# Performance work log

Hardware: AMD Instinct MI355X
Metric: run time of the kernel (lower is better)

## Reference

```python
import jax, jax.numpy as jnp
import numpy as np

EPS = 1e-5
CROSS = 12  # cross_size


def bn(x, g, b):
    # inference BatchNorm2d with running_mean=0, running_var=1
    s = g / jnp.sqrt(1.0 + EPS)
    return x * s[None, :, None, None] + b[None, :, None, None]


def conv1x1(x, w, b=None):
    # w: [out_c, in_c]
    y = jnp.einsum('bchw,oc->bohw', x, w)
    if b is not None:
        y = y + b[None, :, None, None]
    return y


def mlp(x, w1, b1, w2, b2):
    # Mlp with channels_first=True: 1x1 conv -> GELU -> 1x1 conv (drop=0)
    return conv1x1(jax.nn.gelu(conv1x1(x, w1, b1), approximate=False), w2, b2)


def setup_inputs() -> dict:
    key = jax.random.key(0)
    ks = jax.random.split(key, 24)
    B, Cl, Ch = 8, 128, 64
    Hl = Wl = 96
    Hh = Wh = 192

    def w(k, o, i):
        return jax.random.normal(k, (o, i), jnp.float32) / np.float32(np.sqrt(i))

    return {
        'x_l': jax.random.normal(ks[0], (B, Cl, Hl, Wl), jnp.float32),
        'x_h': jax.random.normal(ks[1], (B, Ch, Hh, Wh), jnp.float32),
        # mlp_l (hidden = in = Cl)
        'mlp_l_w1': w(ks[2], Cl, Cl), 'mlp_l_b1': jnp.zeros((Cl,), jnp.float32),
        'mlp_l_w2': w(ks[3], Cl, Cl), 'mlp_l_b2': jnp.zeros((Cl,), jnp.float32),
        # conv_1x1(Cl->Ch) + BN + ReLU
        'conv_w': w(ks[4], Ch, Cl),
        'conv_bn_g': jnp.ones((Ch,), jnp.float32), 'conv_bn_b': jnp.zeros((Ch,), jnp.float32),
        # cross_kv: BN(Cl) -> AdaptiveMaxPool(12,12) -> Conv1x1(Cl -> 2*Ch)
        'kv_bn_g': jnp.ones((Cl,), jnp.float32), 'kv_bn_b': jnp.zeros((Cl,), jnp.float32),
        'kv_w': w(ks[5], 2 * Ch, Cl), 'kv_b': jnp.zeros((2 * Ch,), jnp.float32),
        # self.norm: BN(Ch)
        'norm_g': jnp.ones((Ch,), jnp.float32), 'norm_b': jnp.zeros((Ch,), jnp.float32),
        # mlp_h
        'mlp_h_w1': w(ks[6], Ch, Ch), 'mlp_h_b1': jnp.zeros((Ch,), jnp.float32),
        'mlp_h_w2': w(ks[7], Ch, Ch), 'mlp_h_b2': jnp.zeros((Ch,), jnp.float32),
    }


def reference(x_l, x_h,
              mlp_l_w1, mlp_l_b1, mlp_l_w2, mlp_l_b2,
              conv_w, conv_bn_g, conv_bn_b,
              kv_bn_g, kv_bn_b, kv_w, kv_b,
              norm_g, norm_b,
              mlp_h_w1, mlp_h_b1, mlp_h_w2, mlp_h_b2):
    B, Cl, Hl, Wl = x_l.shape
    _, Ch, Hh, Wh = x_h.shape
    S = CROSS * CROSS  # 144

    # x_l = x_l + mlp_l(x_l)
    x_l = x_l + mlp(x_l, mlp_l_w1, mlp_l_b1, mlp_l_w2, mlp_l_b2)

    # x_h = x_h + interpolate(conv(x_l))
    x_l_conv = jax.nn.relu(bn(conv1x1(x_l, conv_w), conv_bn_g, conv_bn_b))
    up = jax.image.resize(x_l_conv, (B, Ch, Hh, Wh), method='linear')
    x_h = x_h + up

    # cross_kv(x_l): BN -> adaptive max pool to 12x12 -> 1x1 conv to 2*Ch
    xn_l = bn(x_l, kv_bn_g, kv_bn_b)
    pooled = xn_l.reshape(B, Cl, CROSS, Hl // CROSS, CROSS, Wl // CROSS).max(axis=(3, 5))
    kv = conv1x1(pooled, kv_w, kv_b)              # [B, 2*Ch, 12, 12]
    k, v = kv[:, :Ch], kv[:, Ch:]                 # each [B, Ch, 12, 12]
    k_mat = k.transpose(0, 2, 3, 1).reshape(B, S, Ch)  # grouped-conv kernel [B,S,Ch]
    v_mat = v.reshape(B, Ch, S)                        # grouped-conv kernel [B,Ch,S]

    # attn_h
    xn_h = bn(x_h, norm_g, norm_b)                # [B,Ch,Hh,Wh]
    attn = jnp.einsum('bchw,bsc->bshw', xn_h, k_mat)  # [B,S,Hh,Wh]
    attn = jax.nn.softmax(attn * (S ** -0.5), axis=1)
    out = jnp.einsum('bshw,bcs->bchw', attn, v_mat)   # [B,Ch,Hh,Wh]
    x_h = x_h + out

    # x_h = x_h + mlp_h(x_h)
    x_h = x_h + mlp(x_h, mlp_h_w1, mlp_h_b1, mlp_h_w2, mlp_h_b2)
    return x_h
```

## Files before the change

kernel.cpp:

```cpp
#include <hip/hip_runtime.h>
#include <math.h>

#define NB 8
#define CL 128
#define CH 64
#define HL 96
#define WL 96
#define PL (HL*WL)
#define HH 192
#define WH 192
#define PH (HH*WH)
#define NS 144
#define BN_S 0.9999950000374997f
#define INV12 (1.0f/12.0f)

typedef __attribute__((ext_vector_type(8))) short bf16x8;
typedef __attribute__((ext_vector_type(4))) float f32x4;
typedef __attribute__((ext_vector_type(2))) unsigned int uu2;
#define MFMA16(a,b,c) __builtin_amdgcn_mfma_f32_16x16x32_bf16(a,b,c,0,0,0)

__device__ __forceinline__ float gelu_exact(float x){
    return 0.5f*x*(1.0f + erff(x*0.7071067811865475f));
}
__device__ __forceinline__ void st4(short* p, float a, float b, float c, float d){
    uu2 r;
    asm("v_cvt_pk_bf16_f32 %0, %1, %2" : "=v"(r.x) : "v"(a), "v"(b));
    asm("v_cvt_pk_bf16_f32 %0, %1, %2" : "=v"(r.y) : "v"(c), "v"(d));
    *(uu2*)p = r;
}
__device__ __forceinline__ void st4v(short* p, float4 v){ st4(p, v.x, v.y, v.z, v.w); }

__global__ __launch_bounds__(512) void k_mlp_l(
    const float* __restrict__ xl, const float* __restrict__ w1, const float* __restrict__ b1,
    const float* __restrict__ w2, const float* __restrict__ b2,
    const float* __restrict__ cw, const float* __restrict__ bng, const float* __restrict__ bnb,
    float* __restrict__ xl2, float* __restrict__ xc)
{
    __shared__ short Wb[128*136];
    __shared__ short Xb[64*136];
    __shared__ float bS[256];
    __shared__ float bC[128];
    const int tid = threadIdx.x;
    const int b   = blockIdx.x / (PL/64);
    const int hw0 = (blockIdx.x % (PL/64)) * 64;
    const float* xb = xl + (size_t)b*CL*PL + hw0;
    const int w = tid>>6, lane = tid&63, l16 = lane&15, q = lane>>4;
    const int g = w&3, h = w>>2;
    const int pw = g*16, px = pw + l16;
    #pragma unroll
    for (int i=0;i<8;i++){
        int idx4 = i*512+tid;
        int row = idx4>>5, c4 = (idx4&31)<<2;
        st4v(&Wb[row*136 + c4], *(const float4*)&w1[(row<<7) + c4]);
    }
    {
        const int p = tid&63, wv = tid>>6;
        #pragma unroll
        for (int i=0;i<4;i++){
            int c0 = wv*4 + i*32;
            float a0 = xb[(size_t)(c0+0)*PL + p];
            float a1 = xb[(size_t)(c0+1)*PL + p];
            float a2 = xb[(size_t)(c0+2)*PL + p];
            float a3 = xb[(size_t)(c0+3)*PL + p];
            st4(&Xb[p*136 + c0], a0,a1,a2,a3);
        }
    }
    if (tid < 128) bS[tid] = b1[tid]; else if (tid < 256) bS[tid] = b2[tid-128];
    if (tid < 64) bC[tid] = bng[tid]*BN_S; else if (tid < 128) bC[tid] = bnb[tid-64];
    __syncthreads();
    float hv[4][4];
    #pragma unroll
    for (int m2=0; m2<4; m2++){
        const int mt = h*4 + m2;
        f32x4 acc = {0.f,0.f,0.f,0.f};
        #pragma unroll
        for (int k=0;k<4;k++){
            bf16x8 af = *(const bf16x8*)&Wb[(mt*16+l16)*136 + k*32 + q*8];
            bf16x8 bf = *(const bf16x8*)&Xb[(pw+l16)*136 + k*32 + q*8];
            acc = MFMA16(af, bf, acc);
        }
        #pragma unroll
        for (int r=0;r<4;r++) hv[m2][r] = gelu_exact(acc[r] + bS[mt*16+q*4+r]);
    }
    __syncthreads();
    #pragma unroll
    for (int m2=0;m2<4;m2++)
        st4(&Xb[px*136 + (h*4+m2)*16 + q*4], hv[m2][0],hv[m2][1],hv[m2][2],hv[m2][3]);
    #pragma unroll
    for (int i=0;i<8;i++){
        int idx4 = i*512+tid;
        int row = idx4>>5, c4 = (idx4&31)<<2;
        st4v(&Wb[row*136 + c4], *(const float4*)&w2[(row<<7) + c4]);
    }
    __syncthreads();
    float* yb = xl2 + (size_t)b*CL*PL + hw0;
    #pragma unroll
    for (int m2=0; m2<4; m2++){
        const int mt = h*4 + m2;
        f32x4 acc = {0.f,0.f,0.f,0.f};
        #pragma unroll
        for (int k=0;k<4;k++){
            bf16x8 af = *(const bf16x8*)&Wb[(mt*16+l16)*136 + k*32 + q*8];
            bf16x8 bf = *(const bf16x8*)&Xb[(pw+l16)*136 + k*32 + q*8];
            acc = MFMA16(af, bf, acc);
        }
        #pragma unroll
        for (int r=0;r<4;r++){
            int o = mt*16 + q*4 + r;
            size_t off = (size_t)o*PL + px;
            float yy = acc[r] + bS[128+o] + xb[off];
            yb[off] = yy;
            hv[m2][r] = yy;
        }
    }
    __syncthreads();
    #pragma unroll
    for (int m2=0;m2<4;m2++)
        st4(&Xb[px*136 + (h*4+m2)*16 + q*4], hv[m2][0],hv[m2][1],hv[m2][2],hv[m2][3]);
    #pragma unroll
    for (int i=0;i<4;i++){
        int idx4 = i*512+tid;
        int row = idx4>>5, c4 = (idx4&31)<<2;
        st4v(&Wb[row*136 + c4], *(const float4*)&cw[(row<<7) + c4]);
    }
    __syncthreads();
    float* cb = xc + (size_t)b*CH*PL + hw0;
    #pragma unroll
    for (int m2=0; m2<2; m2++){
        const int mt = h*2 + m2;
        f32x4 acc = {0.f,0.f,0.f,0.f};
        #pragma unroll
        for (int k=0;k<4;k++){
            bf16x8 af = *(const bf16x8*)&Wb[(mt*16+l16)*136 + k*32 + q*8];
            bf16x8 bf = *(const bf16x8*)&Xb[(pw+l16)*136 + k*32 + q*8];
            acc = MFMA16(af, bf, acc);
        }
        #pragma unroll
        for (int r=0;r<4;r++){
            int o = mt*16 + q*4 + r;
            cb[(size_t)o*PL + px] = fmaxf(bC[o]*acc[r] + bC[64+o], 0.f);
        }
    }
}

__global__ __launch_bounds__(192) void k_pool(
    const float* __restrict__ xl2, const float* __restrict__ g, const float* __restrict__ bta,
    float* __restrict__ pooled)
{
    const int plane = blockIdx.x;
    const int tid = threadIdx.x;
    if (tid >= NS) return;
    const int c = plane & (CL-1);
    const float sc = g[c]*BN_S;
    const float tc = bta[c];
    const int i = tid/12, j = tid%12;
    const float* base = xl2 + (size_t)plane*PL + (size_t)i*8*WL + j*8;
    float m = -3.4e38f;
    #pragma unroll
    for (int dy=0;dy<8;dy++){
        float4 a = *(const float4*)(base + dy*WL);
        float4 bb = *(const float4*)(base + dy*WL + 4);
        float m0 = fmaxf(fmaxf(sc*a.x+tc, sc*a.y+tc), fmaxf(sc*a.z+tc, sc*a.w+tc));
        float m1 = fmaxf(fmaxf(sc*bb.x+tc, sc*bb.y+tc), fmaxf(sc*bb.z+tc, sc*bb.w+tc));
        m = fmaxf(m, fmaxf(m0, m1));
    }
    pooled[(size_t)plane*NS + tid] = m;
}

__global__ __launch_bounds__(256) void k_kv(
    const float* __restrict__ pooled, const float* __restrict__ kvw, const float* __restrict__ kvb,
    const float* __restrict__ ng, const float* __restrict__ nb,
    float* __restrict__ keg, float* __restrict__ vg, float* __restrict__ biasg)
{
    const int t = blockIdx.x*256 + threadIdx.x;
    const int s = t % NS;
    const int r = t / NS;
    const int o = r & 127;
    const int b = r >> 7;
    const float* P = pooled + (size_t)b*CL*NS + s;
    const float* W = kvw + (size_t)o*CL;
    float acc = kvb[o];
    #pragma unroll 4
    for (int c=0;c<CL;c++) acc = fmaf(W[c], P[(size_t)c*NS], acc);
    if (o < CH){
        keg[((size_t)b*NS+s)*CH + o] = acc * (ng[o]*(BN_S*INV12));
        atomicAdd(&biasg[b*NS+s], acc * (nb[o]*INV12));
    } else {
        vg[((size_t)b*CH + (o-CH))*NS + s] = acc;
    }
}

__global__ __launch_bounds__(256) void k_attn(
    const float* __restrict__ xh, const float* __restrict__ xc,
    const float* __restrict__ keg, const float* __restrict__ vg,
    const float* __restrict__ biasg,
    const float* __restrict__ w1h, const float* __restrict__ b1h,
    const float* __restrict__ w2h, const float* __restrict__ b2h,
    float* __restrict__ out)
{
    __shared__ short KP[64*168];
    __shared__ short VW[64*168];
    __shared__ short Xb[64*72];
    __shared__ float bS[NS];
    __shared__ float bH[128];
    const int tid = threadIdx.x;
    const int b   = blockIdx.x / (PH/64);
    const int hw0 = (blockIdx.x % (PH/64)) * 64;
    const int y   = hw0 / WH;
    const int xst = hw0 % WH;
    const int   lyr = (y>>1) - ((y&1)^1);
    const float fy  = (y&1) ? 0.25f : 0.75f;
    const int   y0i = lyr<0?0:lyr;
    const int   y1i = (lyr+1>HL-1)?(HL-1):(lyr+1);

    const float* xb  = xh + (size_t)b*CH*PH + hw0;
    const float* xcb = xc + (size_t)b*CH*PL;
    const float* keb = keg + (size_t)b*NS*CH;
    const float* vb  = vg + (size_t)b*CH*NS;

    const int w = tid>>6, lane = tid&63, l16 = lane&15, q = lane>>4;
    const int pw = w*16, px = pw + l16;

    #pragma unroll
    for (int i=0;i<9;i++){
        int idx4 = i*256+tid;
        int s = idx4>>4, c4 = (idx4&15)<<2;
        st4v(&KP[s*72 + c4], *(const float4*)&keb[(s<<6) + c4]);
    }
    #pragma unroll
    for (int i=0;i<9;i++){
        int idx4 = i*256+tid;
        int c = idx4/36, s4 = (idx4 - c*36)<<2;
        st4v(&VW[c*168 + s4], *(const float4*)&vb[c*NS + s4]);
    }
    { int row = tid>>2, o4 = (tid&3)<<2;
      *(uu2*)&VW[row*168 + 144 + o4] = (uu2){0u,0u}; }
    if (tid < NS) bS[tid] = biasg[b*NS+tid];
    if (tid < 64) bH[tid] = b1h[tid]; else if (tid < 128) bH[tid] = b2h[tid-64];

    const int xo  = xst + px;
    const int lx  = (xo>>1) - ((xo&1)^1);
    const float fx = (xo&1) ? 0.25f : 0.75f;
    const int x0i = lx<0?0:lx;
    const int x1i = (lx+1>WL-1)?(WL-1):(lx+1);
    float resid[16];
    #pragma unroll
    for (int mt=0; mt<4; mt++){
        #pragma unroll
        for (int r=0; r<4; r++){
            int ch = mt*16 + q*4 + r;
            const float* s = xcb + (size_t)ch*PL;
            float v00 = s[y0i*WL+x0i], v01 = s[y0i*WL+x1i];
            float v10 = s[y1i*WL+x0i], v11 = s[y1i*WL+x1i];
            float top = v00 + fx*(v01-v00);
            float bot = v10 + fx*(v11-v10);
            float up  = top + fy*(bot-top);
            resid[mt*4+r] = xb[(size_t)ch*PH + px] + up;
        }
        st4(&Xb[px*72 + mt*16 + q*4],
            resid[mt*4+0], resid[mt*4+1], resid[mt*4+2], resid[mt*4+3]);
    }
    __syncthreads();

    float ev[9][4];
    float mloc = -3.4e38f;
    #pragma unroll
    for (int st=0; st<9; st++){
        f32x4 acc = {0.f,0.f,0.f,0.f};
        #pragma unroll
        for (int k=0;k<2;k++){
            bf16x8 af = *(const bf16x8*)&KP[(st*16+l16)*72 + k*32 + q*8];
            bf16x8 bf = *(const bf16x8*)&Xb[(pw+l16)*72 + k*32 + q*8];
            acc = MFMA16(af, bf, acc);
        }
        #pragma unroll
        for (int r=0;r<4;r++){
            float v = acc[r] + bS[st*16+q*4+r];
            ev[st][r] = v; mloc = fmaxf(mloc, v);
        }
    }
    mloc = fmaxf(mloc, __shfl_xor(mloc,16));
    mloc = fmaxf(mloc, __shfl_xor(mloc,32));
    float sloc = 0.f;
    #pragma unroll
    for (int st=0;st<9;st++)
        #pragma unroll
        for (int r=0;r<4;r++){ float e = __expf(ev[st][r]-mloc); ev[st][r]=e; sloc+=e; }
    sloc += __shfl_xor(sloc,16);
    sloc += __shfl_xor(sloc,32);
    const float rs = 1.f/sloc;
    __syncthreads();

    #pragma unroll
    for (int st=0;st<9;st++)
        st4(&KP[px*168 + st*16 + q*4], ev[st][0], ev[st][1], ev[st][2], ev[st][3]);
    *(uu2*)&KP[px*168 + 144 + q*4] = (uu2){0u,0u};

    #pragma unroll
    for (int mt=0; mt<4; mt++){
        f32x4 acc = {0.f,0.f,0.f,0.f};
        #pragma unroll
        for (int k=0;k<5;k++){
            bf16x8 af = *(const bf16x8*)&VW[(mt*16+l16)*168 + k*32 + q*8];
            bf16x8 bf = *(const bf16x8*)&KP[(pw+l16)*168 + k*32 + q*8];
            acc = MFMA16(af, bf, acc);
        }
        #pragma unroll
        for (int r=0;r<4;r++)
            resid[mt*4+r] = resid[mt*4+r] + acc[r]*rs;
        st4(&Xb[px*72 + mt*16 + q*4],
            resid[mt*4+0], resid[mt*4+1], resid[mt*4+2], resid[mt*4+3]);
    }
    __syncthreads();

    #pragma unroll
    for (int i=0;i<4;i++){
        int idx4 = i*256+tid;
        int o = idx4>>4, c4 = (idx4&15)<<2;
        st4v(&VW[o*72 + c4], *(const float4*)&w1h[(o<<6) + c4]);
    }
    #pragma unroll
    for (int i=0;i<4;i++){
        int idx4 = i*256+tid;
        int o = idx4>>4, c4 = (idx4&15)<<2;
        st4v(&VW[4608 + o*72 + c4], *(const float4*)&w2h[(o<<6) + c4]);
    }
    __syncthreads();

    float hv[4][4];
    #pragma unroll
    for (int mt=0; mt<4; mt++){
        f32x4 acc = {0.f,0.f,0.f,0.f};
        #pragma unroll
        for (int k=0;k<2;k++){
            bf16x8 af = *(const bf16x8*)&VW[(mt*16+l16)*72 + k*32 + q*8];
            bf16x8 bf = *(const bf16x8*)&Xb[(pw+l16)*72 + k*32 + q*8];
            acc = MFMA16(af, bf, acc);
        }
        #pragma unroll
        for (int r=0;r<4;r++) hv[mt][r] = gelu_exact(acc[r] + bH[mt*16+q*4+r]);
    }
    #pragma unroll
    for (int mt=0;mt<4;mt++)
        st4(&Xb[px*72 + mt*16 + q*4], hv[mt][0], hv[mt][1], hv[mt][2], hv[mt][3]);

    float* ob = out + (size_t)b*CH*PH + hw0;
    #pragma unroll
    for (int mt=0; mt<4; mt++){
        f32x4 acc = {0.f,0.f,0.f,0.f};
        #pragma unroll
        for (int k=0;k<2;k++){
            bf16x8 af = *(const bf16x8*)&VW[4608 + (mt*16+l16)*72 + k*32 + q*8];
            bf16x8 bf = *(const bf16x8*)&Xb[(pw+l16)*72 + k*32 + q*8];
            acc = MFMA16(af, bf, acc);
        }
        #pragma unroll
        for (int r=0;r<4;r++){
            int ch = mt*16 + q*4 + r;
            ob[(size_t)ch*PH + px] = acc[r] + bH[64+ch] + resid[mt*4+r];
        }
    }
}

extern "C" void kernel_launch(void* const* d_in, const int* in_sizes, int n_in,
                              void* d_out, int out_size, void* d_ws, size_t ws_size,
                              hipStream_t stream)
{
    const float* xl    = (const float*)d_in[0];
    const float* xh    = (const float*)d_in[1];
    const float* ml_w1 = (const float*)d_in[2];
    const float* ml_b1 = (const float*)d_in[3];
    const float* ml_w2 = (const float*)d_in[4];
    const float* ml_b2 = (const float*)d_in[5];
    const float* cw    = (const float*)d_in[6];
    const float* cbg   = (const float*)d_in[7];
    const float* cbb   = (const float*)d_in[8];
    const float* kbg   = (const float*)d_in[9];
    const float* kbb   = (const float*)d_in[10];
    const float* kvw   = (const float*)d_in[11];
    const float* kvb   = (const float*)d_in[12];
    const float* ng    = (const float*)d_in[13];
    const float* nb    = (const float*)d_in[14];
    const float* mh_w1 = (const float*)d_in[15];
    const float* mh_b1 = (const float*)d_in[16];
    const float* mh_w2 = (const float*)d_in[17];
    const float* mh_b2 = (const float*)d_in[18];
    float* out = (float*)d_out;

    float* ws     = (float*)d_ws;
    float* xl2    = ws;
    float* xc     = xl2    + (size_t)NB*CL*PL;
    float* pooled = xc     + (size_t)NB*CH*PL;
    float* keg    = pooled + (size_t)NB*CL*NS;
    float* vg     = keg    + (size_t)NB*NS*CH;
    float* biasg  = vg     + (size_t)NB*NS*CH;

    k_mlp_l<<<dim3(NB*PL/64), dim3(512), 0, stream>>>(xl, ml_w1, ml_b1, ml_w2, ml_b2,
                                                      cw, cbg, cbb, xl2, xc);
    k_pool<<<dim3(NB*CL), dim3(192), 0, stream>>>(xl2, kbg, kbb, pooled);
    hipMemsetAsync(biasg, 0, (size_t)NB*NS*sizeof(float), stream);
    k_kv<<<dim3((NB*128*NS)/256), dim3(256), 0, stream>>>(pooled, kvw, kvb, ng, nb, keg, vg, biasg);
    k_attn<<<dim3(NB*PH/64), dim3(256), 0, stream>>>(xh, xc, keg, vg, biasg,
                                                     mh_w1, mh_b1, mh_w2, mh_b2, out);
}
```

Measured before the change: 308.0 us.

## Pass softmax probabilities to PV MFMA via lane shuffles instead of LDS

The softmax exponentials are packed to bf16 in registers and redistributed with cross-lane shuffles into the B-operand layout of the second MFMA, rather than written to shared memory and read back. This removes one __syncthreads and an LDS round trip, and shrinks the K buffer to its actual size. Launch bounds now request 3 blocks per SIMD to raise occupancy. In exchange it adds many shuffle instructions and uses inline asm for the bf16 pack, and the occupancy target may force register spills.

```diff
diff --git a/kernel.cpp b/kernel.cpp
--- a/kernel.cpp
+++ b/kernel.cpp
@@ -190,7 +190,7 @@
     }
 }
 
-__global__ __launch_bounds__(256) void k_attn(
+__global__ __launch_bounds__(256, 3) void k_attn(
     const float* __restrict__ xh, const float* __restrict__ xc,
     const float* __restrict__ keg, const float* __restrict__ vg,
     const float* __restrict__ biasg,
@@ -198,7 +198,7 @@
     const float* __restrict__ w2h, const float* __restrict__ b2h,
     float* __restrict__ out)
 {
-    __shared__ short KP[64*168];
+    __shared__ short Ke[144*72];
     __shared__ short VW[64*168];
     __shared__ short Xb[64*72];
     __shared__ float bS[NS];
@@ -225,7 +225,7 @@
     for (int i=0;i<9;i++){
         int idx4 = i*256+tid;
         int s = idx4>>4, c4 = (idx4&15)<<2;
-        st4v(&KP[s*72 + c4], *(const float4*)&keb[(s<<6) + c4]);
+        st4v(&Ke[s*72 + c4], *(const float4*)&keb[(s<<6) + c4]);
     }
     #pragma unroll
     for (int i=0;i<9;i++){
@@ -269,7 +269,7 @@
         f32x4 acc = {0.f,0.f,0.f,0.f};
         #pragma unroll
         for (int k=0;k<2;k++){
-            bf16x8 af = *(const bf16x8*)&KP[(st*16+l16)*72 + k*32 + q*8];
+            bf16x8 af = *(const bf16x8*)&Ke[(st*16+l16)*72 + k*32 + q*8];
             bf16x8 bf = *(const bf16x8*)&Xb[(pw+l16)*72 + k*32 + q*8];
             acc = MFMA16(af, bf, acc);
         }
@@ -289,25 +289,49 @@
     sloc += __shfl_xor(sloc,16);
     sloc += __shfl_xor(sloc,32);
     const float rs = 1.f/sloc;
-    __syncthreads();
-
-    #pragma unroll
-    for (int st=0;st<9;st++)
-        st4(&KP[px*168 + st*16 + q*4], ev[st][0], ev[st][1], ev[st][2], ev[st][3]);
-    *(uu2*)&KP[px*168 + 144 + q*4] = (uu2){0u,0u};
-
+
+    unsigned pkx[9], pky[9];
+    #pragma unroll
+    for (int st=0; st<9; st++){
+        asm("v_cvt_pk_bf16_f32 %0, %1, %2" : "=v"(pkx[st]) : "v"(ev[st][0]), "v"(ev[st][1]));
+        asm("v_cvt_pk_bf16_f32 %0, %1, %2" : "=v"(pky[st]) : "v"(ev[st][2]), "v"(ev[st][3]));
+    }
+    const int la = ((lane>>4)&1)*32 + l16;
+    const int lb = la + 16;
+    const bool hi = (lane >= 32);
+
+    f32x4 pacc[4];
+    #pragma unroll
+    for (int mt=0;mt<4;mt++) pacc[mt] = (f32x4){0.f,0.f,0.f,0.f};
+    #pragma unroll
+    for (int k=0;k<5;k++){
+        union { unsigned u[4]; bf16x8 v; } pf;
+        if (k<4){
+            unsigned e0 = __shfl(pkx[2*k],   la), o0 = __shfl(pkx[2*k+1], la);
+            unsigned e1 = __shfl(pky[2*k],   la), o1 = __shfl(pky[2*k+1], la);
+            unsigned e2 = __shfl(pkx[2*k],   lb), o2 = __shfl(pkx[2*k+1], lb);
+            unsigned e3 = __shfl(pky[2*k],   lb), o3 = __shfl(pky[2*k+1], lb);
+            pf.u[0] = hi ? o0 : e0;
+            pf.u[1] = hi ? o1 : e1;
+            pf.u[2] = hi ? o2 : e2;
+            pf.u[3] = hi ? o3 : e3;
+        } else {
+            pf.u[0] = __shfl(pkx[8], la);
+            pf.u[1] = __shfl(pky[8], la);
+            pf.u[2] = __shfl(pkx[8], lb);
+            pf.u[3] = __shfl(pky[8], lb);
+        }
+        #pragma unroll
+        for (int mt=0;mt<4;mt++){
+            bf16x8 af = *(const bf16x8*)&VW[(mt*16+l16)*168 + k*32 + q*8];
+            pacc[mt] = MFMA16(af, pf.v, pacc[mt]);
+        }
+    }
     #pragma unroll
     for (int mt=0; mt<4; mt++){
-        f32x4 acc = {0.f,0.f,0.f,0.f};
-        #pragma unroll
-        for (int k=0;k<5;k++){
-            bf16x8 af = *(const bf16x8*)&VW[(mt*16+l16)*168 + k*32 + q*8];
-            bf16x8 bf = *(const bf16x8*)&KP[(pw+l16)*168 + k*32 + q*8];
-            acc = MFMA16(af, bf, acc);
-        }
         #pragma unroll
         for (int r=0;r<4;r++)
-            resid[mt*4+r] = resid[mt*4+r] + acc[r]*rs;
+            resid[mt*4+r] = resid[mt*4+r] + pacc[mt][r]*rs;
         st4(&Xb[px*72 + mt*16 + q*4],
             resid[mt*4+0], resid[mt*4+1], resid[mt*4+2], resid[mt*4+3]);
     }
```

New measurement: 308.5 us. Within noise of the previous version (+0.2%).
